# Kernel optimization log

Measured on AMD Instinct MI355X. Metric: run time of the kernel, lower is better.

Reference implementation:

```python
import jax, jax.numpy as jnp
import numpy as np

VOCAB = 32000
EMB = 512
UNITS = 1024
B, T = 128, 256


def setup_inputs() -> dict:
    key = jax.random.key(0)
    ks = jax.random.split(key, 9)
    s = 0.05
    return {
        "tokens": jax.random.randint(ks[0], (B, T), 0, VOCAB),
        "emb_table": jax.random.normal(ks[1], (VOCAB, EMB), jnp.float32) * s,
        "Wx_f": jax.random.normal(ks[2], (EMB, 3 * UNITS), jnp.float32) * s,
        "Wh_f": jax.random.normal(ks[3], (UNITS, 3 * UNITS), jnp.float32) * s,
        "b_f": jnp.zeros((2, 3 * UNITS), jnp.float32),  # [input_bias, recurrent_bias] (reset_after=True)
        "Wx_b": jax.random.normal(ks[4], (EMB, 3 * UNITS), jnp.float32) * s,
        "Wh_b": jax.random.normal(ks[5], (UNITS, 3 * UNITS), jnp.float32) * s,
        "b_b": jnp.zeros((2, 3 * UNITS), jnp.float32),
        "fc_W": jax.random.normal(ks[6], (2 * UNITS, UNITS), jnp.float32) * s,
        "fc_b": jnp.zeros((UNITS,), jnp.float32),
    }


def _gru_dir(x_proj, mask, Wh, b_rec, reverse):
    # x_proj: [B,T,3U] precomputed input projections (z|r|h gate order, Keras),
    # mask: [B,T] bool. Keras GRU v2 semantics: reset_after=True,
    # sigmoid recurrent activation, tanh activation; masked steps carry state.
    b, u = x_proj.shape[0], Wh.shape[0]

    def step(h, inputs):
        xp, m = inputs  # [B,3U], [B]
        rec = h @ Wh + b_rec  # [B,3U]
        xz, xr, xh = jnp.split(xp, 3, axis=-1)
        rz, rr, rh = jnp.split(rec, 3, axis=-1)
        z = jax.nn.sigmoid(xz + rz)
        r = jax.nn.sigmoid(xr + rr)
        hh = jnp.tanh(xh + r * rh)
        h_new = z * h + (1.0 - z) * hh
        h_new = jnp.where(m[:, None], h_new, h)
        return h_new, h_new

    h0 = jnp.zeros((b, u), x_proj.dtype)
    xs = (jnp.swapaxes(x_proj, 0, 1), jnp.swapaxes(mask, 0, 1))  # time-major
    h_last, outs = jax.lax.scan(step, h0, xs, reverse=reverse)
    return jnp.swapaxes(outs, 0, 1), h_last  # [B,T,U], [B,U]


def reference(tokens, emb_table, Wx_f, Wh_f, b_f, Wx_b, Wh_b, b_b, fc_W, fc_b):
    mask = tokens != 0  # Embedding(mask_zero=True)
    x = emb_table[tokens]  # [B,T,E]
    xp_f = x @ Wx_f + b_f[0]
    xp_b = x @ Wx_b + b_b[0]
    out_f, h_f = _gru_dir(xp_f, mask, Wh_f, b_f[1], reverse=False)
    out_b, h_b = _gru_dir(xp_b, mask, Wh_b, b_b[1], reverse=True)
    output = jnp.concatenate([out_f, out_b], axis=-1)  # [B,T,2U]
    hidden = jnp.concatenate([h_f, h_b], axis=-1) @ fc_W + fc_b  # [B,U]
    return output, hidden
```

## Files before the change

### kernel.cpp

```cpp
#include <hip/hip_runtime.h>


#define T_SEQ 256
#define BATCH 128
#define EMB_D 512
#define UNITS 1024
#define NROWS (BATCH * T_SEQ)
#define N3U 3072
#define N6U 6144
#define XT_STRIDE 786432
#define HSTR (BATCH * 2048)
#define HROT 16

#define SBAR()      __builtin_amdgcn_s_barrier()
#define SCHED0()    __builtin_amdgcn_sched_barrier(0)
#define WAIT_LGKM() asm volatile("s_waitcnt lgkmcnt(0)" ::: "memory")
#define WAIT_VM()   asm volatile("s_waitcnt vmcnt(0)" ::: "memory")

typedef __attribute__((ext_vector_type(8))) __bf16 bfv8;
typedef __attribute__((ext_vector_type(4))) float f32x4;

__device__ inline unsigned short f2bf(float f) {
  union { float f; unsigned int u; } x; x.f = f;
  unsigned int u = x.u;
  unsigned int r = (u + 0x7fffu + ((u >> 16) & 1u)) >> 16;
  return (unsigned short)r;
}
__device__ inline float bf2f(unsigned short h) {
  union { unsigned int u; float f; } x; x.u = ((unsigned int)h) << 16;
  return x.f;
}
__device__ inline f32x4 mfma16(bfv8 a, bfv8 b, f32x4 c) {
  return __builtin_amdgcn_mfma_f32_16x16x32_bf16(a, b, c, 0, 0, 0);
}
__device__ inline void gl_lds16(const unsigned short* g, unsigned short* l) {
  __builtin_amdgcn_global_load_lds(
      (const __attribute__((address_space(1))) void*)g,
      (__attribute__((address_space(3))) void*)l, 16, 0, 0);
}

__global__ __launch_bounds__(256) void k_transpose(const float* __restrict__ src,
                                                   unsigned short* __restrict__ dst,
                                                   int K, int N) {
  __shared__ float tile[32][33];
  int k0 = blockIdx.x * 32, n0 = blockIdx.y * 32;
  int tx = threadIdx.x & 31, ty = threadIdx.x >> 5;
#pragma unroll
  for (int i = 0; i < 4; ++i)
    tile[ty + i * 8][tx] = src[(size_t)(k0 + ty + i * 8) * N + n0 + tx];
  __syncthreads();
#pragma unroll
  for (int i = 0; i < 4; ++i)
    dst[(size_t)(n0 + ty + i * 8) * K + k0 + tx] = f2bf(tile[tx][ty + i * 8]);
}

__global__ __launch_bounds__(256) void k_gather(const int* __restrict__ tokens,
                                                const float* __restrict__ emb,
                                                unsigned short* __restrict__ Xbf) {
  int idx = blockIdx.x * 256 + threadIdx.x;
  int row = idx >> 7;
  int c4 = (idx & 127) * 4;
  int tok = tokens[row];
  float4 v = *(const float4*)(emb + (size_t)tok * EMB_D + c4);
  ushort4 p;
  p.x = f2bf(v.x); p.y = f2bf(v.y); p.z = f2bf(v.z); p.w = f2bf(v.w);
  *(ushort4*)(Xbf + (size_t)row * EMB_D + c4) = p;
}

__global__ __launch_bounds__(256) void k_bias(const float* __restrict__ bf_,
                                              const float* __restrict__ bb_,
                                              float* __restrict__ biasX,
                                              float* __restrict__ biasH) {
  int i = blockIdx.x * 256 + threadIdx.x;
  if (i >= N6U) return;
  if (i < N3U) { biasX[i] = bf_[i];        biasH[i] = bf_[N3U + i]; }
  else         { biasX[i] = bb_[i - N3U];  biasH[i] = bb_[i]; }
}

__global__ __launch_bounds__(256) void k_tokt(const int* __restrict__ tokens,
                                              int* __restrict__ tokT) {
  int i = blockIdx.x * 256 + threadIdx.x;
  int b = i >> 8, t = i & 255;
  tokT[t * BATCH + b] = tokens[i];
}

__global__ __launch_bounds__(256) void k_gemm(const unsigned short* __restrict__ A,
                                              const unsigned short* __restrict__ BT,
                                              const float* __restrict__ bias,
                                              void* __restrict__ C,
                                              int M, int N, int K, int mode) {
  __shared__ unsigned short As[128 * 32];
  __shared__ unsigned short Bs[128 * 32];
  const int mt = blockIdx.x, nt = blockIdx.y;
  const int tid = threadIdx.x;
  const int wid = tid >> 6, lane = tid & 63;
  const int wm = (wid >> 1) * 64, wn = (wid & 1) * 64;
  const int l15 = lane & 15, lk = (lane >> 4) * 8;

  f32x4 acc[4][4];
#pragma unroll
  for (int i = 0; i < 4; ++i)
#pragma unroll
    for (int j = 0; j < 4; ++j) acc[i][j] = (f32x4){0.f, 0.f, 0.f, 0.f};

  const int r = tid >> 2;
  const int cc = (tid & 3) * 8;
  const unsigned short* ga0 = A + (size_t)(mt * 128 + r) * K + cc;
  const unsigned short* ga1 = ga0 + (size_t)64 * K;
  const unsigned short* gb0 = BT + (size_t)(nt * 128 + r) * K + cc;
  const unsigned short* gb1 = gb0 + (size_t)64 * K;
  unsigned short* lA0 = As + r * 32 + cc;
  unsigned short* lA1 = As + (64 + r) * 32 + cc;
  unsigned short* lB0 = Bs + r * 32 + cc;
  unsigned short* lB1 = Bs + (64 + r) * 32 + cc;

  for (int k0 = 0; k0 < K; k0 += 32) {
    __syncthreads();
    gl_lds16(ga0 + k0, lA0);
    gl_lds16(ga1 + k0, lA1);
    gl_lds16(gb0 + k0, lB0);
    gl_lds16(gb1 + k0, lB1);
    __syncthreads();
    bfv8 af[4], bfr[4];
#pragma unroll
    for (int i = 0; i < 4; ++i) {
      af[i]  = *(const bfv8*)(As + (wm + i * 16 + l15) * 32 + lk);
      bfr[i] = *(const bfv8*)(Bs + (wn + i * 16 + l15) * 32 + lk);
    }
#pragma unroll
    for (int i = 0; i < 4; ++i)
#pragma unroll
      for (int j = 0; j < 4; ++j) acc[i][j] = mfma16(af[i], bfr[j], acc[i][j]);
  }

#pragma unroll
  for (int j = 0; j < 4; ++j) {
    const int col = nt * 128 + wn + j * 16 + l15;
    const float bv = bias[col];
    const int dirc = (col >= N3U) ? 1 : 0;
    const int cm = col - dirc * N3U;
    const int g = cm >> 10;
    const int uu = cm & 1023;
    const size_t cbase = (size_t)dirc * 393216 + (size_t)(uu >> 4) * 6144 +
                         (size_t)g * 16 + (uu & 15);
#pragma unroll
    for (int i = 0; i < 4; ++i) {
      const int row0 = mt * 128 + wm + i * 16 + (lane >> 4) * 4;
#pragma unroll
      for (int q = 0; q < 4; ++q) {
        const float v = acc[i][j][q] + bv;
        const int row = row0 + q;
        if (mode == 1) {
          ((float*)C)[(size_t)row * N + col] = v;
        } else {
          const int b = row >> 8, tt = row & 255;
          ((unsigned short*)C)[(size_t)tt * XT_STRIDE + cbase + (size_t)b * 48] = f2bf(v);
        }
      }
    }
  }
}

__global__ __launch_bounds__(256) void k_scan(const unsigned short* __restrict__ XPn,
                                              const unsigned short* __restrict__ WhT,
                                              const float* __restrict__ biasH,
                                              const int* __restrict__ tokT,
                                              unsigned short* __restrict__ hbR,
                                              float* __restrict__ out,
                                              unsigned int* __restrict__ bar) {
  __shared__ unsigned short Wl[3 * 128 * 16 * 8];
  __shared__ unsigned short xb[64 * 48];
  __shared__ int tkb[64];
  __shared__ unsigned short bounce[64 * 24];

  const int bid = blockIdx.x;
  const int grp = bid & 3;
  const int dir = grp >> 1;
  const int mg  = grp & 1;
  const int ut  = bid >> 2;
  const int u0 = ut * 16, m0 = mg * 64;
  const int sub = ut & 7;
  const int tid = threadIdx.x;

  for (int c = tid; c < 6144; c += 256) {
    const int g  = c >> 11;
    const int kb = (c >> 4) & 127;
    const int uu = c & 15;
    *(uint4*)(Wl + (((g << 7) | kb) * 16 + uu) * 8) =
        *(const uint4*)(WhT + (((size_t)(dir * N3U + (g << 10) + u0 + uu)) << 10) + (kb << 3));
  }

  const int lane = tid & 63, wid = tid >> 6;
  const int l15 = lane & 15, hi = lane >> 4;
  const size_t aoff = ((size_t)(m0 + wid * 16 + l15) << 11) + (dir << 10) + (hi << 3);
  const int u = u0 + l15;
  const float bz  = biasH[dir * N3U + u];
  const float brg = biasH[dir * N3U + 1024 + u];
  const float bhg = biasH[dir * N3U + 2048 + u];
  const int rb = wid * 16 + (hi << 2);
  const int ob = m0 + rb;
  const size_t woff = (dir << 10) + u;
  const int sr = tid >> 2, sc4 = (tid & 3) << 2;
  const size_t soff = ((size_t)(m0 + sr) << 11) + (dir << 10) + u0 + sc4;

  unsigned int* genp = &bar[2048 + (grp << 6)];

  const unsigned short* xpb = XPn + (size_t)dir * 393216 + (size_t)ut * 6144 + (size_t)m0 * 48;

  unsigned long long pf0, pf1, pf2; int pft = 0;
  {
    const int t0 = dir ? (T_SEQ - 1) : 0;
    const unsigned long long* xs = (const unsigned long long*)(xpb + (size_t)t0 * XT_STRIDE);
    pf0 = xs[tid]; pf1 = xs[tid + 256]; pf2 = xs[tid + 512];
    if (tid < 64) pft = tokT[t0 * BATCH + m0 + tid];
  }

  float hreg[4] = {0.f, 0.f, 0.f, 0.f};
  float oreg[4];
  __syncthreads();

  for (int s = 0; s < T_SEQ; ++s) {
    const int t = dir ? (T_SEQ - 1 - s) : s;
    const unsigned short* hrd = hbR + (size_t)((s + HROT - 1) & (HROT - 1)) * HSTR;
    unsigned short* hwr       = hbR + (size_t)(s & (HROT - 1)) * HSTR;

    const unsigned short* ap = hrd + aoff;
    bfv8 hA[16], hB[16];
#pragma unroll
    for (int ks = 0; ks < 16; ++ks) {
      hA[ks] = *(const bfv8*)(ap + (ks << 6));
      hB[ks] = *(const bfv8*)(ap + (ks << 6) + 32);
    }

    {
      unsigned long long* xd = (unsigned long long*)xb;
      xd[tid] = pf0; xd[tid + 256] = pf1; xd[tid + 512] = pf2;
      if (tid < 64) tkb[tid] = pft;
    }
    WAIT_LGKM(); SCHED0(); SBAR(); SCHED0();

    float xz[4], xr[4], xh[4]; int tok[4];
#pragma unroll
    for (int q = 0; q < 4; ++q) {
      const int xo = (rb + q) * 48 + l15;
      xz[q] = bf2f(xb[xo]);
      xr[q] = bf2f(xb[xo + 16]);
      xh[q] = bf2f(xb[xo + 32]);
      tok[q] = tkb[rb + q];
    }

    if (s + 1 < T_SEQ) {
      const int tn = dir ? (T_SEQ - 2 - s) : (s + 1);
      const unsigned long long* xs = (const unsigned long long*)(xpb + (size_t)tn * XT_STRIDE);
      pf0 = xs[tid]; pf1 = xs[tid + 256]; pf2 = xs[tid + 512];
      if (tid < 64) pft = tokT[tn * BATCH + m0 + tid];
    }

    f32x4 az0 = {0.f,0.f,0.f,0.f}, az1 = az0, ar0 = az0, ar1 = az0, ah0 = az0, ah1 = az0;
#pragma unroll
    for (int ks = 0; ks < 16; ++ks) {
      const unsigned short* wp = Wl + (((ks << 3) + hi) * 16 + l15) * 8;
      bfv8 wz0 = *(const bfv8*)(wp);
      bfv8 wr0 = *(const bfv8*)(wp + (1 << 14));
      bfv8 wh0 = *(const bfv8*)(wp + (2 << 14));
      bfv8 wz1 = *(const bfv8*)(wp + 512);
      bfv8 wr1 = *(const bfv8*)(wp + (1 << 14) + 512);
      bfv8 wh1 = *(const bfv8*)(wp + (2 << 14) + 512);
      az0 = mfma16(hA[ks], wz0, az0); ar0 = mfma16(hA[ks], wr0, ar0); ah0 = mfma16(hA[ks], wh0, ah0);
      az1 = mfma16(hB[ks], wz1, az1); ar1 = mfma16(hB[ks], wr1, ar1); ah1 = mfma16(hB[ks], wh1, ah1);
    }
    f32x4 az = az0 + az1, ar = ar0 + ar1, ah = ah0 + ah1;

#pragma unroll
    for (int q = 0; q < 4; ++q) {
      const float z  = 1.f / (1.f + __expf(-(xz[q] + az[q] + bz)));
      const float r  = 1.f / (1.f + __expf(-(xr[q] + ar[q] + brg)));
      const float hh = tanhf(xh[q] + r * (ah[q] + bhg));
      float hn = z * hreg[q] + (1.f - z) * hh;
      if (tok[q] == 0) hn = hreg[q];
      hreg[q] = hn;
      oreg[q] = hn;
      bounce[(rb + q) * 24 + l15] = f2bf(hn);
    }

    WAIT_LGKM(); SCHED0(); SBAR(); SCHED0();
    {
      unsigned long long v = *(const unsigned long long*)(bounce + sr * 24 + sc4);
      __hip_atomic_store((unsigned long long*)(hwr + soff), v,
                         __ATOMIC_RELAXED, __HIP_MEMORY_SCOPE_AGENT);
    }

    if (s + 1 < T_SEQ) {
      WAIT_VM(); SCHED0(); SBAR(); SCHED0();
#pragma unroll
      for (int q = 0; q < 4; ++q)
        out[((size_t)((ob + q) * T_SEQ + t) << 11) + woff] = oreg[q];
      if (tid == 0)
        __hip_atomic_fetch_add(&bar[((grp << 3) | sub) << 6], 1u,
                               __ATOMIC_RELAXED, __HIP_MEMORY_SCOPE_AGENT);
      if (ut == 0) {
        if (tid < 8) {
          const unsigned tgt = 8u * (unsigned)(s + 1);
          unsigned int* p = &bar[((grp << 3) | tid) << 6];
          while (__hip_atomic_load(p, __ATOMIC_RELAXED, __HIP_MEMORY_SCOPE_AGENT) < tgt)
            __builtin_amdgcn_s_sleep(2);
        }
        if (tid == 0)
          __hip_atomic_store(genp, (unsigned)(s + 1),
                             __ATOMIC_RELAXED, __HIP_MEMORY_SCOPE_AGENT);
      } else {
        if (tid == 0) {
          const unsigned tgt = (unsigned)(s + 1);
          while (__hip_atomic_load(genp, __ATOMIC_RELAXED, __HIP_MEMORY_SCOPE_AGENT) < tgt)
            __builtin_amdgcn_s_sleep(2);
        }
      }
      if (tid == 0 && ((s & (HROT - 1)) == HROT - 1))
        __builtin_amdgcn_fence(__ATOMIC_ACQUIRE, "agent");
      SBAR(); SCHED0();
    } else {
#pragma unroll
      for (int q = 0; q < 4; ++q)
        out[((size_t)((ob + q) * T_SEQ + t) << 11) + woff] = oreg[q];
    }
  }
}

extern "C" void kernel_launch(void* const* d_in, const int* in_sizes, int n_in,
                              void* d_out, int out_size, void* d_ws, size_t ws_size,
                              hipStream_t stream) {
  const int* tokens = (const int*)d_in[0];
  const float* emb  = (const float*)d_in[1];
  const float* Wx_f = (const float*)d_in[2];
  const float* Wh_f = (const float*)d_in[3];
  const float* b_f  = (const float*)d_in[4];
  const float* Wx_b = (const float*)d_in[5];
  const float* Wh_b = (const float*)d_in[6];
  const float* b_b  = (const float*)d_in[7];
  const float* fc_W = (const float*)d_in[8];
  const float* fc_b = (const float*)d_in[9];
  float* out = (float*)d_out;

  char* w = (char*)d_ws;
  unsigned short* XPn = (unsigned short*)w; w += (size_t)NROWS * N6U * 2;
  unsigned short* Xbf = (unsigned short*)w; w += (size_t)NROWS * EMB_D * 2;
  unsigned short* WxT = (unsigned short*)w; w += (size_t)N6U * EMB_D * 2;
  unsigned short* WhT = (unsigned short*)w; w += (size_t)N6U * UNITS * 2;
  unsigned short* fcWT = (unsigned short*)w; w += (size_t)UNITS * 2048 * 2;
  unsigned short* hbR = (unsigned short*)w; w += (size_t)HROT * HSTR * 2;
  float* biasX = (float*)w; w += N6U * 4;
  float* biasH = (float*)w; w += N6U * 4;
  int* tokT = (int*)w; w += NROWS * 4;
  unsigned int* bar = (unsigned int*)w; w += 4096 * sizeof(unsigned int);

  (void)hipMemsetAsync((void*)(hbR + (size_t)(HROT - 1) * HSTR), 0, (size_t)HSTR * 2, stream);
  (void)hipMemsetAsync((void*)bar, 0, 4096 * sizeof(unsigned int), stream);

  k_transpose<<<dim3(EMB_D / 32, N3U / 32), 256, 0, stream>>>(Wx_f, WxT, EMB_D, N3U);
  k_transpose<<<dim3(EMB_D / 32, N3U / 32), 256, 0, stream>>>(Wx_b, WxT + (size_t)N3U * EMB_D, EMB_D, N3U);
  k_transpose<<<dim3(UNITS / 32, N3U / 32), 256, 0, stream>>>(Wh_f, WhT, UNITS, N3U);
  k_transpose<<<dim3(UNITS / 32, N3U / 32), 256, 0, stream>>>(Wh_b, WhT + (size_t)N3U * UNITS, UNITS, N3U);
  k_transpose<<<dim3(2048 / 32, 1024 / 32), 256, 0, stream>>>(fc_W, fcWT, 2048, 1024);
  k_bias<<<24, 256, 0, stream>>>(b_f, b_b, biasX, biasH);
  k_tokt<<<NROWS / 256, 256, 0, stream>>>(tokens, tokT);
  k_gather<<<(NROWS * 128) / 256, 256, 0, stream>>>(tokens, emb, Xbf);

  k_gemm<<<dim3(NROWS / 128, N6U / 128), 256, 0, stream>>>(Xbf, WxT, biasX, XPn, NROWS, N6U, EMB_D, 0);

  k_scan<<<256, 256, 0, stream>>>(XPn, WhT, biasH, tokT, hbR, out, bar);

  k_gemm<<<dim3(1, 8), 256, 0, stream>>>(hbR + (size_t)(HROT - 1) * HSTR, fcWT, fc_b,
                                         out + (size_t)NROWS * 2048, BATCH, UNITS, 2048, 1);
}
```

Before: 2.330 ms.

## Split recurrent GEMM over K across wave pairs with LDS reduction

```diff
diff --git a/kernel.cpp b/kernel.cpp
--- a/kernel.cpp
+++ b/kernel.cpp
@@ -172,6 +172,7 @@
   __shared__ unsigned short xb[64 * 48];
   __shared__ int tkb[64];
   __shared__ unsigned short bounce[64 * 24];
+  __shared__ float red[2][2][64][13];
 
   const int bid = blockIdx.x;
   const int grp = bid & 3;
@@ -191,14 +192,17 @@
   }
 
   const int lane = tid & 63, wid = tid >> 6;
+  const int kh = wid >> 1, rh = wid & 1;
   const int l15 = lane & 15, hi = lane >> 4;
-  const size_t aoff = ((size_t)(m0 + wid * 16 + l15) << 11) + (dir << 10) + (hi << 3);
+  const size_t aoff0 = ((size_t)(m0 + rh * 32 + l15) << 11) + (dir << 10) + (kh << 9) + (hi << 3);
+  const size_t aoff1 = ((size_t)(m0 + rh * 32 + 16 + l15) << 11) + (dir << 10) + (kh << 9) + (hi << 3);
   const int u = u0 + l15;
   const float bz  = biasH[dir * N3U + u];
   const float brg = biasH[dir * N3U + 1024 + u];
   const float bhg = biasH[dir * N3U + 2048 + u];
-  const int rb = wid * 16 + (hi << 2);
-  const int ob = m0 + rb;
+  const int rb0 = rh * 32 + (hi << 2);
+  const int rb1 = rh * 32 + 16 + (hi << 2);
+  const int ob0 = m0 + rb0, ob1 = m0 + rb1;
   const size_t woff = (dir << 10) + u;
   const int sr = tid >> 2, sc4 = (tid & 3) << 2;
   const size_t soff = ((size_t)(m0 + sr) << 11) + (dir << 10) + u0 + sc4;
@@ -215,8 +219,8 @@
     if (tid < 64) pft = tokT[t0 * BATCH + m0 + tid];
   }
 
-  float hreg[4] = {0.f, 0.f, 0.f, 0.f};
-  float oreg[4];
+  float hreg0[4] = {0.f, 0.f, 0.f, 0.f}, hreg1[4] = {0.f, 0.f, 0.f, 0.f};
+  float oreg0[4], oreg1[4];
   __syncthreads();
 
   for (int s = 0; s < T_SEQ; ++s) {
@@ -224,12 +228,13 @@
     const unsigned short* hrd = hbR + (size_t)((s + HROT - 1) & (HROT - 1)) * HSTR;
     unsigned short* hwr       = hbR + (size_t)(s & (HROT - 1)) * HSTR;
 
-    const unsigned short* ap = hrd + aoff;
+    const unsigned short* ap0 = hrd + aoff0;
+    const unsigned short* ap1 = hrd + aoff1;
     bfv8 hA[16], hB[16];
 #pragma unroll
     for (int ks = 0; ks < 16; ++ks) {
-      hA[ks] = *(const bfv8*)(ap + (ks << 6));
-      hB[ks] = *(const bfv8*)(ap + (ks << 6) + 32);
+      hA[ks] = *(const bfv8*)(ap0 + (ks << 5));
+      hB[ks] = *(const bfv8*)(ap1 + (ks << 5));
     }
 
     {
@@ -238,16 +243,6 @@
       if (tid < 64) tkb[tid] = pft;
     }
     WAIT_LGKM(); SCHED0(); SBAR(); SCHED0();
-
-    float xz[4], xr[4], xh[4]; int tok[4];
-#pragma unroll
-    for (int q = 0; q < 4; ++q) {
-      const int xo = (rb + q) * 48 + l15;
-      xz[q] = bf2f(xb[xo]);
-      xr[q] = bf2f(xb[xo + 16]);
-      xh[q] = bf2f(xb[xo + 32]);
-      tok[q] = tkb[rb + q];
-    }
 
     if (s + 1 < T_SEQ) {
       const int tn = dir ? (T_SEQ - 2 - s) : (s + 1);
@@ -256,31 +251,71 @@
       if (tid < 64) pft = tokT[tn * BATCH + m0 + tid];
     }
 
-    f32x4 az0 = {0.f,0.f,0.f,0.f}, az1 = az0, ar0 = az0, ar1 = az0, ah0 = az0, ah1 = az0;
+    f32x4 az0 = {0.f,0.f,0.f,0.f}, ar0 = az0, ah0 = az0;
+    f32x4 az1 = az0, ar1 = az0, ah1 = az0;
 #pragma unroll
     for (int ks = 0; ks < 16; ++ks) {
-      const unsigned short* wp = Wl + (((ks << 3) + hi) * 16 + l15) * 8;
-      bfv8 wz0 = *(const bfv8*)(wp);
-      bfv8 wr0 = *(const bfv8*)(wp + (1 << 14));
-      bfv8 wh0 = *(const bfv8*)(wp + (2 << 14));
-      bfv8 wz1 = *(const bfv8*)(wp + 512);
-      bfv8 wr1 = *(const bfv8*)(wp + (1 << 14) + 512);
-      bfv8 wh1 = *(const bfv8*)(wp + (2 << 14) + 512);
-      az0 = mfma16(hA[ks], wz0, az0); ar0 = mfma16(hA[ks], wr0, ar0); ah0 = mfma16(hA[ks], wh0, ah0);
-      az1 = mfma16(hB[ks], wz1, az1); ar1 = mfma16(hB[ks], wr1, ar1); ah1 = mfma16(hB[ks], wh1, ah1);
-    }
-    f32x4 az = az0 + az1, ar = ar0 + ar1, ah = ah0 + ah1;
-
-#pragma unroll
-    for (int q = 0; q < 4; ++q) {
-      const float z  = 1.f / (1.f + __expf(-(xz[q] + az[q] + bz)));
-      const float r  = 1.f / (1.f + __expf(-(xr[q] + ar[q] + brg)));
-      const float hh = tanhf(xh[q] + r * (ah[q] + bhg));
-      float hn = z * hreg[q] + (1.f - z) * hh;
-      if (tok[q] == 0) hn = hreg[q];
-      hreg[q] = hn;
-      oreg[q] = hn;
-      bounce[(rb + q) * 24 + l15] = f2bf(hn);
+      const unsigned short* wp = Wl + ((((kh << 6) | (ks << 2) | hi) * 16 + l15) * 8);
+      bfv8 wz = *(const bfv8*)(wp);
+      bfv8 wr = *(const bfv8*)(wp + (1 << 14));
+      bfv8 wh = *(const bfv8*)(wp + (2 << 14));
+      az0 = mfma16(hA[ks], wz, az0); ar0 = mfma16(hA[ks], wr, ar0); ah0 = mfma16(hA[ks], wh, ah0);
+      az1 = mfma16(hB[ks], wz, az1); ar1 = mfma16(hB[ks], wr, ar1); ah1 = mfma16(hB[ks], wh, ah1);
+    }
+
+    if (kh == 1) {
+#pragma unroll
+      for (int j = 0; j < 4; ++j) {
+        red[rh][0][lane][j]     = az0[j];
+        red[rh][0][lane][4 + j] = ar0[j];
+        red[rh][0][lane][8 + j] = ah0[j];
+        red[rh][1][lane][j]     = az1[j];
+        red[rh][1][lane][4 + j] = ar1[j];
+        red[rh][1][lane][8 + j] = ah1[j];
+      }
+    }
+    WAIT_LGKM(); SCHED0(); SBAR(); SCHED0();
+
+    if (kh == 0) {
+#pragma unroll
+      for (int j = 0; j < 4; ++j) {
+        az0[j] += red[rh][0][lane][j];
+        ar0[j] += red[rh][0][lane][4 + j];
+        ah0[j] += red[rh][0][lane][8 + j];
+        az1[j] += red[rh][1][lane][j];
+        ar1[j] += red[rh][1][lane][4 + j];
+        ah1[j] += red[rh][1][lane][8 + j];
+      }
+#pragma unroll
+      for (int q = 0; q < 4; ++q) {
+        const int xo0 = (rb0 + q) * 48 + l15;
+        const float xz = bf2f(xb[xo0]);
+        const float xr = bf2f(xb[xo0 + 16]);
+        const float xh = bf2f(xb[xo0 + 32]);
+        const float z  = 1.f / (1.f + __expf(-(xz + az0[q] + bz)));
+        const float r  = 1.f / (1.f + __expf(-(xr + ar0[q] + brg)));
+        const float hh = tanhf(xh + r * (ah0[q] + bhg));
+        float hn = z * hreg0[q] + (1.f - z) * hh;
+        if (tkb[rb0 + q] == 0) hn = hreg0[q];
+        hreg0[q] = hn;
+        oreg0[q] = hn;
+        bounce[(rb0 + q) * 24 + l15] = f2bf(hn);
+      }
+#pragma unroll
+      for (int q = 0; q < 4; ++q) {
+        const int xo1 = (rb1 + q) * 48 + l15;
+        const float xz = bf2f(xb[xo1]);
+        const float xr = bf2f(xb[xo1 + 16]);
+        const float xh = bf2f(xb[xo1 + 32]);
+        const float z  = 1.f / (1.f + __expf(-(xz + az1[q] + bz)));
+        const float r  = 1.f / (1.f + __expf(-(xr + ar1[q] + brg)));
+        const float hh = tanhf(xh + r * (ah1[q] + bhg));
+        float hn = z * hreg1[q] + (1.f - z) * hh;
+        if (tkb[rb1 + q] == 0) hn = hreg1[q];
+        hreg1[q] = hn;
+        oreg1[q] = hn;
+        bounce[(rb1 + q) * 24 + l15] = f2bf(hn);
+      }
     }
 
     WAIT_LGKM(); SCHED0(); SBAR(); SCHED0();
@@ -292,9 +327,13 @@
 
     if (s + 1 < T_SEQ) {
       WAIT_VM(); SCHED0(); SBAR(); SCHED0();
-#pragma unroll
-      for (int q = 0; q < 4; ++q)
-        out[((size_t)((ob + q) * T_SEQ + t) << 11) + woff] = oreg[q];
+      if (kh == 0) {
+#pragma unroll
+        for (int q = 0; q < 4; ++q) {
+          out[((size_t)((ob0 + q) * T_SEQ + t) << 11) + woff] = oreg0[q];
+          out[((size_t)((ob1 + q) * T_SEQ + t) << 11) + woff] = oreg1[q];
+        }
+      }
       if (tid == 0)
         __hip_atomic_fetch_add(&bar[((grp << 3) | sub) << 6], 1u,
                                __ATOMIC_RELAXED, __HIP_MEMORY_SCOPE_AGENT);
@@ -319,9 +358,13 @@
         __builtin_amdgcn_fence(__ATOMIC_ACQUIRE, "agent");
       SBAR(); SCHED0();
     } else {
-#pragma unroll
-      for (int q = 0; q < 4; ++q)
-        out[((size_t)((ob + q) * T_SEQ + t) << 11) + woff] = oreg[q];
+      if (kh == 0) {
+#pragma unroll
+        for (int q = 0; q < 4; ++q) {
+          out[((size_t)((ob0 + q) * T_SEQ + t) << 11) + woff] = oreg0[q];
+          out[((size_t)((ob1 + q) * T_SEQ + t) << 11) + woff] = oreg1[q];
+        }
+      }
     }
   }
 }
```

After: 2.473 ms. 1.06x slower.
